# Optimization experiments

Measured on AMD Instinct MI355X. Metric: run time of the kernel, lower is better.

Reference implementation:

```python
import jax, jax.numpy as jnp
import numpy as np
from jax import lax

B, S, D, H = 2, 2048, 1024, 16
DEPTH = D // H  # 64


def _leaky(x):
    # tf.keras.layers.ReLU(negative_slope=0.1)
    return jnp.where(x >= 0, x, 0.1 * x)


def _split_heads(x):
    # [B,S,D] -> [B,H,S,DEPTH]
    return x.reshape(B, S, H, DEPTH).transpose(0, 2, 1, 3)


def setup_inputs() -> dict:
    key = jax.random.key(0)
    ks = jax.random.split(key, 8)
    w = lambda k: 0.02 * jax.random.normal(k, (D, D), dtype=jnp.float32)
    return {
        "q": jax.random.normal(ks[0], (B, S, D), dtype=jnp.float32),
        "k": jax.random.normal(ks[1], (B, S, D), dtype=jnp.float32),
        "v": jax.random.normal(ks[2], (B, S, D), dtype=jnp.float32),
        "query_mask": jnp.ones((B, S, 1), dtype=jnp.float32),
        "key_mask": jnp.ones((B, S, 1), dtype=jnp.float32),
        "value_mask": jnp.ones((B, S, 1), dtype=jnp.float32),
        "Wq": w(ks[3]), "bq": 0.5 * jnp.ones((D,), dtype=jnp.float32),
        "Wk": w(ks[4]), "bk": 0.5 * jnp.ones((D,), dtype=jnp.float32),
        "Wv": w(ks[5]), "bv": jnp.zeros((D,), dtype=jnp.float32),
        "Wo": w(ks[6]), "bo": jnp.zeros((D,), dtype=jnp.float32),
    }


def _causal_linear_attn(qh, kh, vh):
    # qh,kh,vh: [B,H,S,DEPTH]. Sequential recurrence:
    #   S_t = S_{t-1} + k_t v_t^T ; z_t = z_{t-1} + k_t
    #   out_t = (q_t @ S_t) / (q_t . z_t)
    def step(carry, x):
        S_st, z = carry
        qi, ki, vi = x  # each [B,H,DEPTH]
        S_st = S_st + ki[..., :, None] * vi[..., None, :]  # [B,H,DEPTH,DEPTH]
        z = z + ki
        num = jnp.einsum('bhd,bhde->bhe', qi, S_st)
        den = jnp.einsum('bhd,bhd->bh', qi, z)
        return (S_st, z), num / den[..., None]

    init = (jnp.zeros((B, H, DEPTH, DEPTH), dtype=qh.dtype),
            jnp.zeros((B, H, DEPTH), dtype=qh.dtype))
    xs = (jnp.moveaxis(qh, 2, 0), jnp.moveaxis(kh, 2, 0), jnp.moveaxis(vh, 2, 0))
    _, out = lax.scan(step, init, xs)  # [S,B,H,DEPTH]
    return jnp.moveaxis(out, 0, 2)  # [B,H,S,DEPTH]


def reference(q, k, v, query_mask, key_mask, value_mask,
              Wq, bq, Wk, bk, Wv, bv, Wo, bo):
    q = (q * query_mask) @ Wq + bq
    k = (k * key_mask) @ Wk + bk
    v = (v * value_mask) @ Wv + bv
    q = _leaky(q)
    k = _leaky(k)
    qh, kh, vh = _split_heads(q), _split_heads(k), _split_heads(v)
    attn = _causal_linear_attn(qh, kh, vh)  # [B,H,S,DEPTH]
    concat = attn.transpose(0, 2, 1, 3).reshape(B, S, D)
    return concat @ Wo + bo
```

## Files before the change

### kernel.cpp

```cpp
#include <hip/hip_runtime.h>

#define Bx    2
#define Sx    2048
#define Dx    1024
#define Hx    16
#define NCx   (Sx/64)
#define BHx   (Bx*Hx)
#define Mx    (Bx*Sx)

typedef float    f4 __attribute__((ext_vector_type(4)));
typedef _Float16 h8 __attribute__((ext_vector_type(8)));
typedef _Float16 h4 __attribute__((ext_vector_type(4)));

__device__ __forceinline__ void gl2lds16(const _Float16* g, _Float16* l) {
  __builtin_amdgcn_global_load_lds(
      (const __attribute__((address_space(1))) void*)g,
      (__attribute__((address_space(3))) void*)l, 16, 0, 0);
}

__global__ __launch_bounds__(256) void convert_in(
    const float* __restrict__ q, const float* __restrict__ k,
    const float* __restrict__ v, const float* __restrict__ qm,
    const float* __restrict__ km, const float* __restrict__ vm,
    _Float16* __restrict__ qh, _Float16* __restrict__ kh,
    _Float16* __restrict__ vh)
{
  const int z = blockIdx.y;
  const float* x = (z == 0) ? q : (z == 1) ? k : v;
  const float* m = (z == 0) ? qm : (z == 1) ? km : vm;
  _Float16*    o = (z == 0) ? qh : (z == 1) ? kh : vh;
  const int i4 = blockIdx.x * 256 + threadIdx.x;
  const f4 vv = *(const f4*)(x + (size_t)i4 * 4);
  const float mf = m[i4 >> 8];
  h4 r;
  r[0] = (_Float16)(vv[0] * mf);
  r[1] = (_Float16)(vv[1] * mf);
  r[2] = (_Float16)(vv[2] * mf);
  r[3] = (_Float16)(vv[3] * mf);
  *(h4*)(o + (size_t)i4 * 4) = r;
}

__global__ __launch_bounds__(256) void convert_w(
    const float* __restrict__ W0, const float* __restrict__ W1,
    const float* __restrict__ W2, const float* __restrict__ W3,
    _Float16* __restrict__ T0, _Float16* __restrict__ T1,
    _Float16* __restrict__ T2, _Float16* __restrict__ T3)
{
  const float* W = (blockIdx.z == 0) ? W0 : (blockIdx.z == 1) ? W1 :
                   (blockIdx.z == 2) ? W2 : W3;
  _Float16* T = (blockIdx.z == 0) ? T0 : (blockIdx.z == 1) ? T1 :
                (blockIdx.z == 2) ? T2 : T3;
  __shared__ float Ws[64 * 68];
  const int tx = threadIdx.x & 15, ty = threadIdx.x >> 4;
  const int k0 = blockIdx.y * 64, n0 = blockIdx.x * 64;
#pragma unroll
  for (int i = 0; i < 4; i++) {
    const int r = ty + 16 * i;
    *(f4*)&Ws[r * 68 + tx * 4] = *(const f4*)&W[(size_t)(k0 + r) * Dx + n0 + tx * 4];
  }
  __syncthreads();
#pragma unroll
  for (int i = 0; i < 4; i++) {
    const int n = ty + 16 * i;
    h4 o;
#pragma unroll
    for (int j = 0; j < 4; j++) o[j] = (_Float16)Ws[(tx * 4 + j) * 68 + n];
    *(h4*)&T[(size_t)(n0 + n) * Dx + k0 + tx * 4] = o;
  }
}

struct GArgs {
  const _Float16* A; const _Float16* Bt; const float* bias;
  void* out; int leaky, half_out;
};

template<int BN, int WR, int WC>
__global__ __launch_bounds__(512, 4) void gemm_f16(GArgs g0, GArgs g1, GArgs g2)
{
  const GArgs g = (blockIdx.z == 0) ? g0 : (blockIdx.z == 1) ? g1 : g2;
  constexpr int FM = 128 / WR / 16;
  constexpr int FN = BN / WC / 16;
  __shared__ _Float16 As[128 * 64];
  __shared__ _Float16 Bs[BN * 64];
  const int tid = threadIdx.x;
  const int m0 = blockIdx.y * 128, n0 = blockIdx.x * BN;
  const int lane = tid & 63, wave = tid >> 6;
  const int lm = lane & 15, qd = lane >> 4;
  const int wr = wave % WR, wc = wave / WR;
  const int wm0 = wr * (128 / WR), wn0 = wc * (BN / WC);
  const int srow = lane >> 3;
  const int sseg = (lane & 7) ^ srow;
  const _Float16* gA = g.A  + (size_t)(m0 + srow) * Dx + sseg * 8;
  const _Float16* gB = g.Bt + (size_t)(n0 + srow) * Dx + sseg * 8;

  f4 acc[FM][FN];
#pragma unroll
  for (int i = 0; i < FM; i++)
#pragma unroll
    for (int j = 0; j < FN; j++) { f4 z = {0.f, 0.f, 0.f, 0.f}; acc[i][j] = z; }

  for (int kt = 0; kt < Dx; kt += 64) {
    __syncthreads();
#pragma unroll
    for (int u = 0; u < 2; u++) {
      const int t = wave * 2 + u;
      gl2lds16(gA + (size_t)(t * 8) * Dx + kt, &As[t * 512]);
    }
#pragma unroll
    for (int u = 0; u < BN / 64; u++) {
      const int t = wave * (BN / 64) + u;
      gl2lds16(gB + (size_t)(t * 8) * Dx + kt, &Bs[t * 512]);
    }
    __syncthreads();
#pragma unroll
    for (int kk = 0; kk < 2; kk++) {
      const int sp = ((kk * 4 + qd) ^ (lm & 7)) * 8;
      h8 af[FM];
#pragma unroll
      for (int i = 0; i < FM; i++)
        af[i] = *(const h8*)&As[(wm0 + i * 16 + lm) * 64 + sp];
#pragma unroll
      for (int j = 0; j < FN; j++) {
        const h8 bf = *(const h8*)&Bs[(wn0 + j * 16 + lm) * 64 + sp];
#pragma unroll
        for (int i = 0; i < FM; i++)
          acc[i][j] = __builtin_amdgcn_mfma_f32_16x16x32_f16(af[i], bf, acc[i][j], 0, 0, 0);
      }
    }
  }

#pragma unroll
  for (int j = 0; j < FN; j++) {
    const int n = n0 + wn0 + j * 16 + lm;
    const float bz = g.bias[n];
#pragma unroll
    for (int i = 0; i < FM; i++) {
      const int mb = m0 + wm0 + i * 16 + qd * 4;
#pragma unroll
      for (int r = 0; r < 4; r++) {
        float v = acc[i][j][r] + bz;
        if (g.leaky) v = (v >= 0.f) ? v : 0.1f * v;
        if (g.half_out) ((_Float16*)g.out)[(size_t)(mb + r) * Dx + n] = (_Float16)v;
        else            ((float*)g.out)[(size_t)(mb + r) * Dx + n] = v;
      }
    }
  }
}

__global__ __launch_bounds__(256) void chunkkv_mfma(
    const _Float16* __restrict__ kp, const _Float16* __restrict__ vp,
    _Float16* __restrict__ ckvh, float* __restrict__ cz)
{
  __shared__ _Float16 Kt[64 * 64];
  __shared__ _Float16 Vt[64 * 64];
  const int blk = blockIdx.x;
  const int c = blk & (NCx - 1);
  const int bh = blk / NCx;
  const int b = bh / Hx, h = bh % Hx;
  const int tid = threadIdx.x;
  const size_t rowbase = ((size_t)(b * Sx + c * 64)) * Dx + h * 64;

#pragma unroll
  for (int p = 0; p < 2; p++) {
    const int f = tid + 256 * p;
    const int s = f >> 3, g8 = f & 7;
    const h8 hk = *(const h8*)&kp[rowbase + (size_t)s * Dx + g8 * 8];
    const h8 hv = *(const h8*)&vp[rowbase + (size_t)s * Dx + g8 * 8];
#pragma unroll
    for (int i = 0; i < 8; i++) {
      const int r = g8 * 8 + i;
      const int a = r * 64 + (((s >> 3) ^ (r & 7)) * 8) + (s & 7);
      Kt[a] = hk[i];
      Vt[a] = hv[i];
    }
  }
  __syncthreads();

  const int lane = tid & 63, w = tid >> 6;
  const int lm = lane & 15, qd = lane >> 4;
  const int x7 = lm & 7;

  h8 av[2];
#pragma unroll
  for (int kk = 0; kk < 2; kk++)
    av[kk] = *(const h8*)&Vt[(w * 16 + lm) * 64 + (((kk << 2) + qd) ^ x7) * 8];

#pragma unroll
  for (int dt = 0; dt < 4; dt++) {
    f4 acc = {0.f, 0.f, 0.f, 0.f};
#pragma unroll
    for (int kk = 0; kk < 2; kk++) {
      const h8 bf = *(const h8*)&Kt[(dt * 16 + lm) * 64 + (((kk << 2) + qd) ^ x7) * 8];
      acc = __builtin_amdgcn_mfma_f32_16x16x32_f16(av[kk], bf, acc, 0, 0, 0);
    }
#pragma unroll
    for (int r = 0; r < 4; r++) {
      const int e = w * 16 + qd * 4 + r;
      ckvh[(size_t)blk * 4096 + e * 64 + dt * 16 + lm] = (_Float16)acc[r];
    }
  }

  {
    const int d = tid >> 2, fr = tid & 3;
    float dp = 0.f;
#pragma unroll
    for (int j = 0; j < 2; j++) {
      const h8 kv = *(const h8*)&Kt[d * 64 + (fr * 2 + j) * 8];
#pragma unroll
      for (int i = 0; i < 8; i++) dp += (float)kv[i];
    }
    dp += __shfl_xor(dp, 1);
    dp += __shfl_xor(dp, 2);
    if (fr == 0) cz[(size_t)blk * 64 + d] = dp;
  }
}

__global__ __launch_bounds__(256) void prefix_kernel(
    _Float16* __restrict__ ckvh, float* __restrict__ cz)
{
  const int gid = blockIdx.x * 256 + threadIdx.x;
  const int bh = gid >> 12, el = gid & 4095;
  const size_t base = (((size_t)bh * NCx) << 12) + el;
  float vals[NCx];
#pragma unroll
  for (int c = 0; c < NCx; c++)
    vals[c] = (float)ckvh[base + ((size_t)c << 12)];
  float acc = 0.f;
#pragma unroll
  for (int c = 0; c < NCx; c++) { const float t = vals[c]; vals[c] = acc; acc += t; }
#pragma unroll
  for (int c = 0; c < NCx; c++)
    ckvh[base + ((size_t)c << 12)] = (_Float16)vals[c];

  if (gid < BHx * 64) {
    const int zbh = gid >> 6, d = gid & 63;
    const size_t zb = (size_t)zbh * NCx * 64 + d;
    float zv[NCx];
#pragma unroll
    for (int c = 0; c < NCx; c++) zv[c] = cz[zb + (size_t)c * 64];
    float az = 0.f;
#pragma unroll
    for (int c = 0; c < NCx; c++) { const float t = zv[c]; zv[c] = az; az += t; }
#pragma unroll
    for (int c = 0; c < NCx; c++) cz[zb + (size_t)c * 64] = zv[c];
  }
}

__global__ __launch_bounds__(256) void attn_mfma(
    const _Float16* __restrict__ qp, const _Float16* __restrict__ kp,
    const _Float16* __restrict__ vp, const _Float16* __restrict__ ckvh,
    const float* __restrict__ cz, _Float16* __restrict__ concat)
{
  __shared__ _Float16 Qs[64 * 64];
  __shared__ _Float16 Ks[64 * 64];
  __shared__ _Float16 Vt[64 * 64];
  __shared__ _Float16 Sh[64 * 64];
  __shared__ float zs[64];
  __shared__ float den[64];
  const int blk = blockIdx.x;
  const int c = blk & (NCx - 1);
  const int bh = blk / NCx;
  const int b = bh / Hx, h = bh % Hx;
  const int tid = threadIdx.x;
  const size_t rowbase = ((size_t)(b * Sx + c * 64)) * Dx + h * 64;

#pragma unroll
  for (int p = 0; p < 2; p++) {
    const int f = tid + 256 * p;
    const int r = f >> 3, sg = f & 7;
    const int ph = (sg ^ (r & 7)) * 8;
    *(h8*)&Qs[r * 64 + ph] = *(const h8*)&qp[rowbase + (size_t)r * Dx + sg * 8];
    *(h8*)&Ks[r * 64 + ph] = *(const h8*)&kp[rowbase + (size_t)r * Dx + sg * 8];
    *(h8*)&Sh[r * 64 + ph] = *(const h8*)&ckvh[(size_t)blk * 4096 + r * 64 + sg * 8];
  }
#pragma unroll
  for (int p = 0; p < 2; p++) {
    const int f = tid + 256 * p;
    const int s = f >> 3, g8 = f & 7;
    const h8 hv = *(const h8*)&vp[rowbase + (size_t)s * Dx + g8 * 8];
#pragma unroll
    for (int i = 0; i < 8; i++) {
      const int e = g8 * 8 + i;
      Vt[e * 64 + (((s >> 3) ^ (e & 7)) * 8) + (s & 7)] = hv[i];
    }
  }
  if (tid < 64) zs[tid] = cz[(size_t)blk * 64 + tid];
  __syncthreads();

  const int lane = tid & 63, w = tid >> 6;
  const int lm = lane & 15, qd = lane >> 4;
  const int x7 = lm & 7;

  h8 aq[2];
#pragma unroll
  for (int kk = 0; kk < 2; kk++)
    aq[kk] = *(const h8*)&Qs[(w * 16 + lm) * 64 + (((kk << 2) + qd) ^ x7) * 8];

  f4 pc[4];
#pragma unroll
  for (int st = 0; st < 4; st++) {
    f4 z4 = {0.f, 0.f, 0.f, 0.f}; pc[st] = z4;
#pragma unroll
    for (int kk = 0; kk < 2; kk++) {
      const h8 bf = *(const h8*)&Ks[(st * 16 + lm) * 64 + (((kk << 2) + qd) ^ x7) * 8];
      pc[st] = __builtin_amdgcn_mfma_f32_16x16x32_f16(aq[kk], bf, pc[st], 0, 0, 0);
    }
  }
  float rsum[4] = {0.f, 0.f, 0.f, 0.f};
#pragma unroll
  for (int st = 0; st < 4; st++) {
    const int s = st * 16 + lm;
#pragma unroll
    for (int r = 0; r < 4; r++) {
      const int t = w * 16 + qd * 4 + r;
      float v = pc[st][r];
      v = (s <= t) ? v : 0.f;
      pc[st][r] = v;
      rsum[r] += v;
    }
  }
#pragma unroll
  for (int r = 0; r < 4; r++) {
    rsum[r] += __shfl_xor(rsum[r], 1);
    rsum[r] += __shfl_xor(rsum[r], 2);
    rsum[r] += __shfl_xor(rsum[r], 4);
    rsum[r] += __shfl_xor(rsum[r], 8);
  }
  {
    const int t = tid >> 2, fr = tid & 3;
    float dp = 0.f;
#pragma unroll
    for (int j = 0; j < 2; j++) {
      const int sg = fr * 2 + j;
      const h8 qv = *(const h8*)&Qs[t * 64 + (sg ^ (t & 7)) * 8];
#pragma unroll
      for (int i = 0; i < 8; i++) dp += (float)qv[i] * zs[sg * 8 + i];
    }
    dp += __shfl_xor(dp, 1);
    dp += __shfl_xor(dp, 2);
    if (fr == 0) den[t] = dp;
  }
  __syncthreads();

  _Float16* Pa = Ks;
#pragma unroll
  for (int st = 0; st < 4; st++) {
#pragma unroll
    for (int r = 0; r < 4; r++) {
      const int row = w * 16 + qd * 4 + r;
      Pa[row * 64 + (((st * 2 + (lm >> 3)) ^ (row & 7)) * 8) + (lm & 7)] =
          (_Float16)pc[st][r];
    }
  }
  if (lm == 0) {
#pragma unroll
    for (int r = 0; r < 4; r++) den[w * 16 + qd * 4 + r] += rsum[r];
  }
  __syncthreads();

  h8 ap[2];
#pragma unroll
  for (int kk = 0; kk < 2; kk++)
    ap[kk] = *(const h8*)&Pa[(w * 16 + lm) * 64 + (((kk << 2) + qd) ^ x7) * 8];

  f4 acc[4];
#pragma unroll
  for (int et = 0; et < 4; et++) {
    f4 z4 = {0.f, 0.f, 0.f, 0.f}; acc[et] = z4;
#pragma unroll
    for (int kk = 0; kk < 2; kk++) {
      const h8 bv = *(const h8*)&Vt[(et * 16 + lm) * 64 + (((kk << 2) + qd) ^ x7) * 8];
      acc[et] = __builtin_amdgcn_mfma_f32_16x16x32_f16(ap[kk], bv, acc[et], 0, 0, 0);
    }
#pragma unroll
    for (int kk = 0; kk < 2; kk++) {
      const h8 bs = *(const h8*)&Sh[(et * 16 + lm) * 64 + (((kk << 2) + qd) ^ x7) * 8];
      acc[et] = __builtin_amdgcn_mfma_f32_16x16x32_f16(aq[kk], bs, acc[et], 0, 0, 0);
    }
  }

#pragma unroll
  for (int r = 0; r < 4; r++) {
    const int row = w * 16 + qd * 4 + r;
    const float inv = 1.f / den[row];
    _Float16* orow = &concat[((size_t)(b * Sx + c * 64 + row)) * Dx + h * 64];
#pragma unroll
    for (int et = 0; et < 4; et++)
      orow[et * 16 + lm] = (_Float16)(acc[et][r] * inv);
  }
}

extern "C" void kernel_launch(void* const* d_in, const int* in_sizes, int n_in,
                              void* d_out, int out_size, void* d_ws, size_t ws_size,
                              hipStream_t stream)
{
  const float* q  = (const float*)d_in[0];
  const float* k  = (const float*)d_in[1];
  const float* v  = (const float*)d_in[2];
  const float* qm = (const float*)d_in[3];
  const float* km = (const float*)d_in[4];
  const float* vm = (const float*)d_in[5];
  const float* Wq = (const float*)d_in[6];
  const float* bq = (const float*)d_in[7];
  const float* Wk = (const float*)d_in[8];
  const float* bk = (const float*)d_in[9];
  const float* Wv = (const float*)d_in[10];
  const float* bv = (const float*)d_in[11];
  const float* Wo = (const float*)d_in[12];
  const float* bo = (const float*)d_in[13];
  float* out = (float*)d_out;

  char* ws = (char*)d_ws;
  _Float16* qh  = (_Float16*)(ws);
  _Float16* kh  = (_Float16*)(ws + 8388608);
  _Float16* vh  = (_Float16*)(ws + 16777216);
  _Float16* Wtq = (_Float16*)(ws + 25165824);
  _Float16* Wtk = (_Float16*)(ws + 27262976);
  _Float16* Wtv = (_Float16*)(ws + 29360128);
  _Float16* Wto = (_Float16*)(ws + 31457280);
  _Float16* qp  = (_Float16*)(ws + 33554432);
  _Float16* kp  = (_Float16*)(ws + 41943040);
  _Float16* vp  = (_Float16*)(ws + 50331648);
  float*    cz  = (float*)   (ws + 58720256);
  _Float16* ckvh   = qh;
  _Float16* concat = kh;

  convert_in<<<dim3(4096, 3), 256, 0, stream>>>(q, k, v, qm, km, vm, qh, kh, vh);
  convert_w<<<dim3(16, 16, 4), 256, 0, stream>>>(Wq, Wk, Wv, Wo, Wtq, Wtk, Wtv, Wto);

  GArgs gq = { qh, Wtq, bq, qp, 1, 1 };
  GArgs gk = { kh, Wtk, bk, kp, 1, 1 };
  GArgs gv = { vh, Wtv, bv, vp, 0, 1 };
  gemm_f16<128, 4, 2><<<dim3(Dx / 128, Mx / 128, 3), 512, 0, stream>>>(gq, gk, gv);

  chunkkv_mfma<<<BHx * NCx, 256, 0, stream>>>(kp, vp, ckvh, cz);
  prefix_kernel<<<512, 256, 0, stream>>>(ckvh, cz);
  attn_mfma<<<BHx * NCx, 256, 0, stream>>>(qp, kp, vp, ckvh, cz, concat);

  GArgs go = { concat, Wto, bo, out, 0, 0 };
  gemm_f16<64, 4, 2><<<dim3(Dx / 64, Mx / 128, 1), 512, 0, stream>>>(go, go, go);
}
```

Before: 201.7 us.

## Widen input conversion, add second-level LDS swizzle, and raise MFMA priority

The input conversion kernel now handles 8 elements per thread with 16-byte fp16 stores and launches half as many blocks. The transposed K/V tiles in LDS get an extra XOR term from the row's upper bits, meant to cut bank conflicts on the scalar transpose writes; all readers of those tiles are updated to match. s_setprio is placed around the MFMA loops in the chunk and attention kernels so those waves get issue priority. These are small kernels, so any gain is likely minor, and the index math adds a few ALU ops.

```diff
diff --git a/kernel.cpp b/kernel.cpp
--- a/kernel.cpp
+++ b/kernel.cpp
@@ -29,15 +29,17 @@
   const float* x = (z == 0) ? q : (z == 1) ? k : v;
   const float* m = (z == 0) ? qm : (z == 1) ? km : vm;
   _Float16*    o = (z == 0) ? qh : (z == 1) ? kh : vh;
-  const int i4 = blockIdx.x * 256 + threadIdx.x;
-  const f4 vv = *(const f4*)(x + (size_t)i4 * 4);
-  const float mf = m[i4 >> 8];
-  h4 r;
-  r[0] = (_Float16)(vv[0] * mf);
-  r[1] = (_Float16)(vv[1] * mf);
-  r[2] = (_Float16)(vv[2] * mf);
-  r[3] = (_Float16)(vv[3] * mf);
-  *(h4*)(o + (size_t)i4 * 4) = r;
+  const int i8 = blockIdx.x * 256 + threadIdx.x;
+  const f4 v0 = *(const f4*)(x + (size_t)i8 * 8);
+  const f4 v1 = *(const f4*)(x + (size_t)i8 * 8 + 4);
+  const float mf = m[i8 >> 7];
+  h8 r;
+#pragma unroll
+  for (int i = 0; i < 4; i++) {
+    r[i]     = (_Float16)(v0[i] * mf);
+    r[4 + i] = (_Float16)(v1[i] * mf);
+  }
+  *(h8*)(o + (size_t)i8 * 8) = r;
 }
 
 __global__ __launch_bounds__(256) void convert_w(
@@ -169,7 +171,7 @@
 #pragma unroll
     for (int i = 0; i < 8; i++) {
       const int r = g8 * 8 + i;
-      const int a = r * 64 + (((s >> 3) ^ (r & 7)) * 8) + (s & 7);
+      const int a = r * 64 + ((((s >> 3) ^ (r & 7)) ^ ((r >> 3) & 7)) * 8) + (s & 7);
       Kt[a] = hk[i];
       Vt[a] = hv[i];
     }
@@ -178,19 +180,25 @@
 
   const int lane = tid & 63, w = tid >> 6;
   const int lm = lane & 15, qd = lane >> 4;
-  const int x7 = lm & 7;
 
   h8 av[2];
-#pragma unroll
-  for (int kk = 0; kk < 2; kk++)
-    av[kk] = *(const h8*)&Vt[(w * 16 + lm) * 64 + (((kk << 2) + qd) ^ x7) * 8];
-
+  {
+    const int rv = w * 16 + lm;
+    const int xv = (rv & 7) ^ ((rv >> 3) & 7);
+#pragma unroll
+    for (int kk = 0; kk < 2; kk++)
+      av[kk] = *(const h8*)&Vt[rv * 64 + ((((kk << 2) + qd)) ^ xv) * 8];
+  }
+
+  __builtin_amdgcn_s_setprio(1);
 #pragma unroll
   for (int dt = 0; dt < 4; dt++) {
+    const int rk = dt * 16 + lm;
+    const int xk = (rk & 7) ^ ((rk >> 3) & 7);
     f4 acc = {0.f, 0.f, 0.f, 0.f};
 #pragma unroll
     for (int kk = 0; kk < 2; kk++) {
-      const h8 bf = *(const h8*)&Kt[(dt * 16 + lm) * 64 + (((kk << 2) + qd) ^ x7) * 8];
+      const h8 bf = *(const h8*)&Kt[rk * 64 + ((((kk << 2) + qd)) ^ xk) * 8];
       acc = __builtin_amdgcn_mfma_f32_16x16x32_f16(av[kk], bf, acc, 0, 0, 0);
     }
 #pragma unroll
@@ -199,13 +207,15 @@
       ckvh[(size_t)blk * 4096 + e * 64 + dt * 16 + lm] = (_Float16)acc[r];
     }
   }
+  __builtin_amdgcn_s_setprio(0);
 
   {
     const int d = tid >> 2, fr = tid & 3;
+    const int dx = (d & 7) ^ ((d >> 3) & 7);
     float dp = 0.f;
 #pragma unroll
     for (int j = 0; j < 2; j++) {
-      const h8 kv = *(const h8*)&Kt[d * 64 + (fr * 2 + j) * 8];
+      const h8 kv = *(const h8*)&Kt[d * 64 + ((fr * 2 + j) ^ dx) * 8];
 #pragma unroll
       for (int i = 0; i < 8; i++) dp += (float)kv[i];
     }
@@ -281,7 +291,7 @@
 #pragma unroll
     for (int i = 0; i < 8; i++) {
       const int e = g8 * 8 + i;
-      Vt[e * 64 + (((s >> 3) ^ (e & 7)) * 8) + (s & 7)] = hv[i];
+      Vt[e * 64 + ((((s >> 3) ^ (e & 7)) ^ ((e >> 3) & 7)) * 8) + (s & 7)] = hv[i];
     }
   }
   if (tid < 64) zs[tid] = cz[(size_t)blk * 64 + tid];
@@ -297,6 +307,7 @@
     aq[kk] = *(const h8*)&Qs[(w * 16 + lm) * 64 + (((kk << 2) + qd) ^ x7) * 8];
 
   f4 pc[4];
+  __builtin_amdgcn_s_setprio(1);
 #pragma unroll
   for (int st = 0; st < 4; st++) {
     f4 z4 = {0.f, 0.f, 0.f, 0.f}; pc[st] = z4;
@@ -306,6 +317,7 @@
       pc[st] = __builtin_amdgcn_mfma_f32_16x16x32_f16(aq[kk], bf, pc[st], 0, 0, 0);
     }
   }
+  __builtin_amdgcn_s_setprio(0);
   float rsum[4] = {0.f, 0.f, 0.f, 0.f};
 #pragma unroll
   for (int st = 0; st < 4; st++) {
@@ -364,20 +376,24 @@
     ap[kk] = *(const h8*)&Pa[(w * 16 + lm) * 64 + (((kk << 2) + qd) ^ x7) * 8];
 
   f4 acc[4];
+  __builtin_amdgcn_s_setprio(1);
 #pragma unroll
   for (int et = 0; et < 4; et++) {
+    const int re = et * 16 + lm;
+    const int xv = (re & 7) ^ ((re >> 3) & 7);
     f4 z4 = {0.f, 0.f, 0.f, 0.f}; acc[et] = z4;
 #pragma unroll
     for (int kk = 0; kk < 2; kk++) {
-      const h8 bv = *(const h8*)&Vt[(et * 16 + lm) * 64 + (((kk << 2) + qd) ^ x7) * 8];
+      const h8 bv = *(const h8*)&Vt[re * 64 + ((((kk << 2) + qd)) ^ xv) * 8];
       acc[et] = __builtin_amdgcn_mfma_f32_16x16x32_f16(ap[kk], bv, acc[et], 0, 0, 0);
     }
 #pragma unroll
     for (int kk = 0; kk < 2; kk++) {
-      const h8 bs = *(const h8*)&Sh[(et * 16 + lm) * 64 + (((kk << 2) + qd) ^ x7) * 8];
+      const h8 bs = *(const h8*)&Sh[re * 64 + (((kk << 2) + qd) ^ x7) * 8];
       acc[et] = __builtin_amdgcn_mfma_f32_16x16x32_f16(aq[kk], bs, acc[et], 0, 0, 0);
     }
   }
+  __builtin_amdgcn_s_setprio(0);
 
 #pragma unroll
   for (int r = 0; r < 4; r++) {
@@ -425,7 +441,7 @@
   _Float16* ckvh   = qh;
   _Float16* concat = kh;
 
-  convert_in<<<dim3(4096, 3), 256, 0, stream>>>(q, k, v, qm, km, vm, qh, kh, vh);
+  convert_in<<<dim3(2048, 3), 256, 0, stream>>>(q, k, v, qm, km, vm, qh, kh, vh);
   convert_w<<<dim3(16, 16, 4), 256, 0, stream>>>(Wq, Wk, Wv, Wo, Wtq, Wtk, Wtv, Wto);
 
   GArgs gq = { qh, Wtq, bq, qp, 1, 1 };
```

Measured after the change: 202.9 us. About the same (+0.6%).
